# Kernel tuning notes

Measured on AMD Instinct MI355X. Metric: run time of the kernel, lower is better.

Reference implementation:

```python
import jax, jax.numpy as jnp
import numpy as np

D = 768
H = 8
DH = D // H
SCALE = DH ** -0.5


def layer_norm(x, g, b, eps=1e-5):
    mu = jnp.mean(x, axis=-1, keepdims=True)
    var = jnp.var(x, axis=-1, keepdims=True)
    return (x - mu) * jax.lax.rsqrt(var + eps) * g + b


def setup_inputs() -> dict:
    key = jax.random.key(0)
    ks = jax.random.split(key, 8)
    B, N = 8, 1024
    s = lambda fan_in: 1.0 / np.sqrt(fan_in)
    return {
        "x": jax.random.normal(ks[0], (B, N, D), jnp.float32),
        "w_qkv": jax.random.normal(ks[1], (D, 3 * D), jnp.float32) * s(D),
        "w_o": jax.random.normal(ks[2], (D, D), jnp.float32) * s(D),
        "b_o": jnp.zeros((D,), jnp.float32),
        "w1": jax.random.normal(ks[3], (D, 4 * D), jnp.float32) * s(D),
        "b1": jnp.zeros((4 * D,), jnp.float32),
        "w2": jax.random.normal(ks[4], (4 * D, D), jnp.float32) * s(4 * D),
        "b2": jnp.zeros((D,), jnp.float32),
        "g1": jnp.ones((D,), jnp.float32), "be1": jnp.zeros((D,), jnp.float32),
        "gm": jnp.ones((D,), jnp.float32), "bm": jnp.zeros((D,), jnp.float32),
        "g3": jnp.ones((D,), jnp.float32), "be3": jnp.zeros((D,), jnp.float32),
    }


def reference(x, w_qkv, w_o, b_o, w1, b1, w2, b2, g1, be1, gm, bm, g3, be3):
    B, N, _ = x.shape
    # --- attention branch (pre-norm) ---
    h = layer_norm(x, g1, be1)
    qkv = h @ w_qkv                                   # (B,N,3D)
    qkv = qkv.reshape(B, N, 3, H, DH).transpose(2, 0, 3, 1, 4)  # (3,B,H,N,Dh)
    q, k, v = qkv[0], qkv[1], qkv[2]
    att = jax.nn.softmax(jnp.einsum('bhnd,bhmd->bhnm', q, k) * SCALE, axis=-1)
    o = jnp.einsum('bhnm,bhmd->bhnd', att, v)         # (B,H,N,Dh)
    # faithful to original: reshape WITHOUT transposing heads back
    o = o.reshape(B, N, D)
    o = o @ w_o + b_o
    x = o + x
    # --- MLP branch (has its own pre-norm; GELU after BOTH linears; dropout off) ---
    h = layer_norm(x, gm, bm)
    h = jax.nn.gelu(h @ w1 + b1, approximate=False)
    h = jax.nn.gelu(h @ w2 + b2, approximate=False)
    x = h + x
    return layer_norm(x, g3, be3)
```

## Files before the change

### kernel.cpp

```cpp
#include <hip/hip_runtime.h>
#include <cmath>
#include <cstdint>

typedef __bf16 bf16;
typedef __bf16 bf16x8 __attribute__((ext_vector_type(8)));
typedef __bf16 bf16x4 __attribute__((ext_vector_type(4)));
typedef float  f32x4  __attribute__((ext_vector_type(4)));

#define M_TOK 8192
#define SCALE_ 0.10206207261596575f

__device__ __forceinline__ void gld_lds16(const void* g, void* l) {
  __builtin_amdgcn_global_load_lds(
      (__attribute__((address_space(1))) void*)(uintptr_t)g,
      (__attribute__((address_space(3))) void*)(uintptr_t)l,
      16, 0, 0);
}

__device__ __forceinline__ float gelu_f(float x) {
  float u = x * (0.7978845608f + 0.0356774081f * x * x);
  float t = 1.0f - 2.0f / (__expf(2.0f * u) + 1.0f);
  return 0.5f * x * (1.0f + t);
}

__global__ __launch_bounds__(256) void make_frags_kernel(
    const float* __restrict__ w_qkv, const float* __restrict__ w_o,
    const float* __restrict__ w1, const float* __restrict__ w2,
    bf16* __restrict__ fqkv, bf16* __restrict__ fwo, bf16* __restrict__ fw1,
    bf16* __restrict__ fw2) {
  int chunk = blockIdx.x * 4 + (threadIdx.x >> 6);
  int lane = threadIdx.x & 63;
  const float* src;
  bf16* dst;
  int K, N, base;
  if (chunk < 3456) {
    src = w_qkv; dst = fqkv; K = 768; N = 2304; base = 0;
  } else if (chunk < 4608) {
    src = w_o; dst = fwo; K = 768; N = 768; base = 3456;
  } else if (chunk < 9216) {
    src = w1; dst = fw1; K = 768; N = 3072; base = 4608;
  } else {
    src = w2; dst = fw2; K = 3072; N = 768; base = 9216;
  }
  int lid = chunk - base;
  int kc = K / 32;
  int n16 = lid / kc, c = lid - n16 * kc;
  int lr = lane & 15, qd = lane >> 4;
  int n = n16 * 16 + lr;
  int k0 = c * 32 + qd * 8;
  bf16x8 v;
#pragma unroll
  for (int e = 0; e < 8; e++) v[e] = (bf16)src[(size_t)(k0 + e) * N + n];
  *(bf16x8*)&dst[(size_t)lid * 512 + lane * 8] = v;
}

__global__ __launch_bounds__(256) void ln_kernel(
    const float* __restrict__ x, const float* __restrict__ g,
    const float* __restrict__ b, bf16* __restrict__ ob) {
  int w = threadIdx.x >> 6, lane = threadIdx.x & 63;
  size_t row = (size_t)blockIdx.x * 4 + w;
  const float* xr = x + row * 768;
  float4 v[3];
  float s = 0.f, sq = 0.f;
#pragma unroll
  for (int k = 0; k < 3; k++) {
    v[k] = *(const float4*)(xr + (k * 64 + lane) * 4);
    s += v[k].x + v[k].y + v[k].z + v[k].w;
    sq += v[k].x * v[k].x + v[k].y * v[k].y + v[k].z * v[k].z + v[k].w * v[k].w;
  }
#pragma unroll
  for (int off = 32; off >= 1; off >>= 1) {
    s += __shfl_xor(s, off);
    sq += __shfl_xor(sq, off);
  }
  float mean = s * (1.f / 768.f);
  float rstd = rsqrtf(sq * (1.f / 768.f) - mean * mean + 1e-5f);
#pragma unroll
  for (int k = 0; k < 3; k++) {
    int c = (k * 64 + lane) * 4;
    float4 gg = *(const float4*)(g + c);
    float4 bb = *(const float4*)(b + c);
    bf16x4 pk = {(bf16)((v[k].x - mean) * rstd * gg.x + bb.x),
                 (bf16)((v[k].y - mean) * rstd * gg.y + bb.y),
                 (bf16)((v[k].z - mean) * rstd * gg.z + bb.z),
                 (bf16)((v[k].w - mean) * rstd * gg.w + bb.w)};
    *(bf16x4*)(ob + row * 768 + c) = pk;
  }
}

__global__ __launch_bounds__(256) void ln2_reduce_kernel(
    const bf16* __restrict__ p, const float* __restrict__ bo,
    const float* __restrict__ xres, const float* __restrict__ g,
    const float* __restrict__ b, bf16* __restrict__ x2,
    bf16* __restrict__ h2) {
  int w = threadIdx.x >> 6, lane = threadIdx.x & 63;
  size_t row = (size_t)blockIdx.x * 4 + w;
  const bf16* p0 = p + row * 768;
  const bf16* p1 = p0 + (size_t)M_TOK * 768;
  const float* xr = xres + row * 768;
  float4 v[3];
  float s = 0.f, sq = 0.f;
#pragma unroll
  for (int k = 0; k < 3; k++) {
    int c = (k * 64 + lane) * 4;
    bf16x4 a0 = *(const bf16x4*)(p0 + c);
    bf16x4 a1 = *(const bf16x4*)(p1 + c);
    float4 bb = *(const float4*)(bo + c);
    float4 rr = *(const float4*)(xr + c);
    v[k].x = (float)a0[0] + (float)a1[0] + bb.x + rr.x;
    v[k].y = (float)a0[1] + (float)a1[1] + bb.y + rr.y;
    v[k].z = (float)a0[2] + (float)a1[2] + bb.z + rr.z;
    v[k].w = (float)a0[3] + (float)a1[3] + bb.w + rr.w;
    bf16x4 xo = {(bf16)v[k].x, (bf16)v[k].y, (bf16)v[k].z, (bf16)v[k].w};
    *(bf16x4*)(x2 + row * 768 + c) = xo;
    s += v[k].x + v[k].y + v[k].z + v[k].w;
    sq += v[k].x * v[k].x + v[k].y * v[k].y + v[k].z * v[k].z + v[k].w * v[k].w;
  }
#pragma unroll
  for (int off = 32; off >= 1; off >>= 1) {
    s += __shfl_xor(s, off);
    sq += __shfl_xor(sq, off);
  }
  float mean = s * (1.f / 768.f);
  float rstd = rsqrtf(sq * (1.f / 768.f) - mean * mean + 1e-5f);
#pragma unroll
  for (int k = 0; k < 3; k++) {
    int c = (k * 64 + lane) * 4;
    float4 gg = *(const float4*)(g + c);
    float4 bb = *(const float4*)(b + c);
    bf16x4 pk = {(bf16)((v[k].x - mean) * rstd * gg.x + bb.x),
                 (bf16)((v[k].y - mean) * rstd * gg.y + bb.y),
                 (bf16)((v[k].z - mean) * rstd * gg.z + bb.z),
                 (bf16)((v[k].w - mean) * rstd * gg.w + bb.w)};
    *(bf16x4*)(h2 + row * 768 + c) = pk;
  }
}

__global__ __launch_bounds__(256) void ln3_reduce_kernel(
    const bf16* __restrict__ p, const float* __restrict__ b2,
    const bf16* __restrict__ x2, const float* __restrict__ g,
    const float* __restrict__ b, float* __restrict__ out) {
  int w = threadIdx.x >> 6, lane = threadIdx.x & 63;
  size_t row = (size_t)blockIdx.x * 4 + w;
  const bf16* p0 = p + row * 768;
  const bf16* p1 = p0 + (size_t)M_TOK * 768;
  const bf16* xr = x2 + row * 768;
  float4 v[3];
  float s = 0.f, sq = 0.f;
#pragma unroll
  for (int k = 0; k < 3; k++) {
    int c = (k * 64 + lane) * 4;
    bf16x4 a0 = *(const bf16x4*)(p0 + c);
    bf16x4 a1 = *(const bf16x4*)(p1 + c);
    float4 bb = *(const float4*)(b2 + c);
    bf16x4 rr = *(const bf16x4*)(xr + c);
    v[k].x = gelu_f((float)a0[0] + (float)a1[0] + bb.x) + (float)rr[0];
    v[k].y = gelu_f((float)a0[1] + (float)a1[1] + bb.y) + (float)rr[1];
    v[k].z = gelu_f((float)a0[2] + (float)a1[2] + bb.z) + (float)rr[2];
    v[k].w = gelu_f((float)a0[3] + (float)a1[3] + bb.w) + (float)rr[3];
    s += v[k].x + v[k].y + v[k].z + v[k].w;
    sq += v[k].x * v[k].x + v[k].y * v[k].y + v[k].z * v[k].z + v[k].w * v[k].w;
  }
#pragma unroll
  for (int off = 32; off >= 1; off >>= 1) {
    s += __shfl_xor(s, off);
    sq += __shfl_xor(sq, off);
  }
  float mean = s * (1.f / 768.f);
  float rstd = rsqrtf(sq * (1.f / 768.f) - mean * mean + 1e-5f);
#pragma unroll
  for (int k = 0; k < 3; k++) {
    int c = (k * 64 + lane) * 4;
    float4 gg = *(const float4*)(g + c);
    float4 bb = *(const float4*)(b + c);
    float4 ov = {(v[k].x - mean) * rstd * gg.x + bb.x,
                 (v[k].y - mean) * rstd * gg.y + bb.y,
                 (v[k].z - mean) * rstd * gg.z + bb.z,
                 (v[k].w - mean) * rstd * gg.w + bb.w};
    *(float4*)(out + row * 768 + c) = ov;
  }
}

template <int EPI, int LDA, int KTOT, int KSL, int NN>
__global__ __launch_bounds__(512, 2) void gemm8p_kernel(
    const bf16* __restrict__ A, const bf16* __restrict__ Bf,
    const float* __restrict__ bias, bf16* __restrict__ outb,
    bf16* __restrict__ qo, bf16* __restrict__ ko, bf16* __restrict__ vto) {
  constexpr int KCg = KTOT / 32;
  constexpr int NT = KSL / 64;
  __shared__ __align__(16) bf16 smem[3][24576];
  int tid = threadIdx.x;
  int w = tid >> 6, l = tid & 63;
  int qd = l >> 4, lr = l & 15;
  int bm0 = blockIdx.x * 128, bn0 = blockIdx.y * 256;
  int kbase = blockIdx.z * KSL;
  int wm = (w >> 2) * 64;
  int wnl = (w & 3) * 4;

  int rA = w * 8 + (l >> 3);
  int csA = (l & 7) ^ (l >> 3);
  const bf16* pA =
      A + (size_t)(bm0 + rA) * LDA + kbase + csA * 8;
  const bf16* pB0 =
      Bf + ((size_t)((bn0 >> 4) + (w >> 1)) * KCg + (kbase >> 5) + (w & 1)) *
               512 +
      l * 8;

  auto STG_A = [&](int t, bf16* buf) {
    gld_lds16(pA + t * 64, (char*)buf + w * 1024);
    gld_lds16(pA + t * 64 + (size_t)64 * LDA, (char*)buf + (8 + w) * 1024);
  };
  auto STG_B = [&](int t, bf16* buf, int g) {
    gld_lds16(pB0 + (size_t)g * (4 * KCg * 512) + (size_t)t * 1024,
              (char*)buf + 16384 + (w + 8 * g) * 1024);
  };

  STG_A(0, smem[0]);
  STG_B(0, smem[0], 0); STG_B(0, smem[0], 1);
  STG_B(0, smem[0], 2); STG_B(0, smem[0], 3);
  STG_A(1, smem[1]);
  STG_B(1, smem[1], 0); STG_B(1, smem[1], 1);
  STG_B(1, smem[1], 2); STG_B(1, smem[1], 3);
  asm volatile("s_waitcnt vmcnt(6)" ::: "memory");
  __builtin_amdgcn_sched_barrier(0);
  __builtin_amdgcn_s_barrier();

  f32x4 acc[4][4] = {};

#pragma unroll 1
  for (int kt3 = 0; kt3 < NT; kt3 += 3) {
#pragma unroll
    for (int u = 0; u < 3; ++u) {
      const int kt = kt3 + u;
      const bf16* Ab = smem[u];
      const bf16* Bb = smem[u] + 8192;
      bf16* nbuf = smem[(u + 2) % 3];
      bool st = (kt + 2) < NT;
#pragma unroll
      for (int k2 = 0; k2 < 2; ++k2) {
        bf16x8 af[4], bv[4];
#pragma unroll
        for (int i = 0; i < 4; ++i)
          af[i] = *(const bf16x8*)(Ab + (wm + i * 16 + lr) * 64 +
                                   (((k2 << 2) | qd) ^ (lr & 7)) * 8);
#pragma unroll
        for (int j = 0; j < 4; ++j)
          bv[j] = *(const bf16x8*)(Bb + (((wnl + j) << 1) | k2) * 512 + l * 8);
        if (k2 == 0) {
          if (st) { STG_A(kt + 2, nbuf); STG_B(kt + 2, nbuf, 0); }
        } else {
          if (st) {
            STG_B(kt + 2, nbuf, 1);
            STG_B(kt + 2, nbuf, 2);
            STG_B(kt + 2, nbuf, 3);
          }
        }
        __builtin_amdgcn_s_barrier();
        asm volatile("s_waitcnt lgkmcnt(0)" ::: "memory");
        __builtin_amdgcn_sched_barrier(0);
        __builtin_amdgcn_s_setprio(1);
#pragma unroll
        for (int i = 0; i < 4; ++i)
#pragma unroll
          for (int j = 0; j < 4; ++j)
            acc[i][j] = __builtin_amdgcn_mfma_f32_16x16x32_bf16(
                af[i], bv[j], acc[i][j], 0, 0, 0);
        __builtin_amdgcn_s_setprio(0);
      }
      if (kt + 1 < NT) {
        if (st) asm volatile("s_waitcnt vmcnt(6)" ::: "memory");
        else    asm volatile("s_waitcnt vmcnt(0)" ::: "memory");
        __builtin_amdgcn_sched_barrier(0);
        __builtin_amdgcn_s_barrier();
      }
    }
  }

  int wn = (w & 3) * 64;
  bf16* outbs = (EPI == 5) ? outb + (size_t)blockIdx.z * M_TOK * NN : outb;

#pragma unroll
  for (int i = 0; i < 4; i++) {
#pragma unroll
    for (int j = 0; j < 4; j++) {
      if (EPI == 4) {
        int colt = bn0 + wn + j * 16;
        int which = colt / 768;
        int rem = colt - which * 768;
        int h = rem / 96;
        int dhb = rem - h * 96;
        int row0 = bm0 + wm + i * 16 + qd * 4;
        int b = row0 >> 10, n0 = row0 & 1023;
        int bh = b * 8 + h;
        if (which == 2) {
          bf16x4 pk = {(bf16)acc[i][j][0], (bf16)acc[i][j][1],
                       (bf16)acc[i][j][2], (bf16)acc[i][j][3]};
          *(bf16x4*)(vto + ((size_t)(bh * 96 + dhb + lr)) * 1024 + n0) = pk;
        } else if (which == 0) {
#pragma unroll
          for (int r = 0; r < 4; r++)
            qo[((size_t)bh * 1024 + n0 + r) * 96 + dhb + lr] =
                (bf16)(acc[i][j][r] * SCALE_);
        } else {
#pragma unroll
          for (int r = 0; r < 4; r++)
            ko[((size_t)bh * 1024 + n0 + r) * 96 + dhb + lr] =
                (bf16)acc[i][j][r];
        }
      } else {
#pragma unroll
        for (int r = 0; r < 4; r++) {
          int row = bm0 + wm + i * 16 + qd * 4 + r;
          int col = bn0 + wn + j * 16 + lr;
          size_t o = (size_t)row * NN + col;
          float v = acc[i][j][r];
          if (EPI == 2) {
            outbs[o] = (bf16)gelu_f(v + bias[col]);
          } else {
            outbs[o] = (bf16)v;
          }
        }
      }
    }
  }
}

__global__ __launch_bounds__(256) void attn_kernel(
    const bf16* __restrict__ qb, const bf16* __restrict__ kb,
    const bf16* __restrict__ vtb, bf16* __restrict__ operm) {
  __shared__ __align__(16) bf16 Ks[2][64 * 104];
  __shared__ __align__(16) bf16 Vs[2][96 * 72];
  __shared__ __align__(16) bf16 Ps[128 * 72];
  int t = threadIdx.x;
  int w = t >> 6, lane = t & 63;
  int qd = lane >> 4, lr = lane & 15;
  int bh = blockIdx.x, nt0 = blockIdx.y * 128;
  int bq = bh >> 3, hh = bh & 7;

  const bf16* kgb = kb + (size_t)bh * 1024 * 96;
  const bf16* vgb = vtb + (size_t)bh * 96 * 1024;

  bf16x8 kreg[3], vreg[3];
#pragma unroll
  for (int it = 0; it < 3; it++) {
    int idx = it * 256 + t;
    kreg[it] = *(const bf16x8*)(kgb + (idx / 12) * 96 + (idx % 12) * 8);
    vreg[it] = *(const bf16x8*)(vgb + (size_t)(idx >> 3) * 1024 + (idx & 7) * 8);
  }

  const bf16* qg = qb + ((size_t)bh * 1024 + nt0 + w * 32) * 96;
  bf16x8 afq[2][3];
#pragma unroll
  for (int i = 0; i < 2; i++)
#pragma unroll
    for (int ks = 0; ks < 3; ks++)
      afq[i][ks] = *(const bf16x8*)(qg + (i * 16 + lr) * 96 + ks * 32 + qd * 8);

  f32x4 oacc[2][6] = {};
  float lst[2][4] = {};

  int cur = 0;
  for (int kt = 0; kt < 16; kt++) {
#pragma unroll
    for (int it = 0; it < 3; it++) {
      int idx = it * 256 + t;
      *(bf16x8*)&Ks[cur][(idx / 12) * 104 + (idx % 12) * 8] = kreg[it];
      *(bf16x8*)&Vs[cur][(idx >> 3) * 72 + (idx & 7) * 8] = vreg[it];
    }
    if (kt < 15) {
      const bf16* kg = kgb + (size_t)(kt + 1) * 64 * 96;
      const bf16* vg = vgb + (kt + 1) * 64;
#pragma unroll
      for (int it = 0; it < 3; it++) {
        int idx = it * 256 + t;
        kreg[it] = *(const bf16x8*)(kg + (idx / 12) * 96 + (idx % 12) * 8);
        vreg[it] =
            *(const bf16x8*)(vg + (size_t)(idx >> 3) * 1024 + (idx & 7) * 8);
      }
    }
    __syncthreads();

    f32x4 sacc[2][4] = {};
#pragma unroll
    for (int ks = 0; ks < 3; ks++) {
      bf16x8 bk[4];
#pragma unroll
      for (int jn = 0; jn < 4; jn++)
        bk[jn] =
            *(const bf16x8*)&Ks[cur][(jn * 16 + lr) * 104 + ks * 32 + qd * 8];
#pragma unroll
      for (int i = 0; i < 2; i++)
#pragma unroll
        for (int jn = 0; jn < 4; jn++)
          sacc[i][jn] = __builtin_amdgcn_mfma_f32_16x16x32_bf16(
              afq[i][ks], bk[jn], sacc[i][jn], 0, 0, 0);
    }

#pragma unroll
    for (int i = 0; i < 2; i++)
#pragma unroll
      for (int jn = 0; jn < 4; jn++)
#pragma unroll
        for (int r = 0; r < 4; r++) {
          float p = __expf(sacc[i][jn][r]);
          lst[i][r] += p;
          Ps[(w * 32 + i * 16 + qd * 4 + r) * 72 + jn * 16 + lr] = (bf16)p;
        }

#pragma unroll
    for (int ks = 0; ks < 2; ks++) {
      bf16x8 ap[2];
#pragma unroll
      for (int i = 0; i < 2; i++)
        ap[i] =
            *(const bf16x8*)&Ps[(w * 32 + i * 16 + lr) * 72 + ks * 32 + qd * 8];
#pragma unroll
      for (int jn = 0; jn < 6; jn++) {
        bf16x8 bv =
            *(const bf16x8*)&Vs[cur][(jn * 16 + lr) * 72 + ks * 32 + qd * 8];
#pragma unroll
        for (int i = 0; i < 2; i++)
          oacc[i][jn] = __builtin_amdgcn_mfma_f32_16x16x32_bf16(
              ap[i], bv, oacc[i][jn], 0, 0, 0);
      }
    }
    cur ^= 1;
  }

#pragma unroll
  for (int i = 0; i < 2; i++)
#pragma unroll
    for (int r = 0; r < 4; r++) {
#pragma unroll
      for (int off = 1; off < 16; off <<= 1)
        lst[i][r] += __shfl_xor(lst[i][r], off);
    }

#pragma unroll
  for (int i = 0; i < 2; i++) {
#pragma unroll
    for (int r = 0; r < 4; r++) {
      float inv = 1.0f / lst[i][r];
      int n = nt0 + w * 32 + i * 16 + qd * 4 + r;
      size_t rowo = (size_t)bq * 1024 + hh * 128 + (n >> 3);
      int colb = 96 * (n & 7);
#pragma unroll
      for (int jn = 0; jn < 6; jn++)
        operm[rowo * 768 + colb + jn * 16 + lr] =
            (bf16)(oacc[i][jn][r] * inv);
    }
  }
}

extern "C" void kernel_launch(void* const* d_in, const int* in_sizes, int n_in,
                              void* d_out, int out_size, void* d_ws,
                              size_t ws_size, hipStream_t stream) {
  const float* x = (const float*)d_in[0];
  const float* w_qkv = (const float*)d_in[1];
  const float* w_o = (const float*)d_in[2];
  const float* b_o = (const float*)d_in[3];
  const float* w1 = (const float*)d_in[4];
  const float* b1 = (const float*)d_in[5];
  const float* w2 = (const float*)d_in[6];
  const float* b2 = (const float*)d_in[7];
  const float* g1 = (const float*)d_in[8];
  const float* be1 = (const float*)d_in[9];
  const float* gm = (const float*)d_in[10];
  const float* bm = (const float*)d_in[11];
  const float* g3 = (const float*)d_in[12];
  const float* be3 = (const float*)d_in[13];

  char* ws = (char*)d_ws;
  size_t off = 0;
  auto alloc = [&](size_t bytes) {
    char* p = ws + off;
    off += (bytes + 255) & ~(size_t)255;
    return p;
  };
  const size_t SZ_TOK_BF = (size_t)M_TOK * 768 * 2;
  bf16* fqkv = (bf16*)alloc((size_t)2304 * 768 * 2);
  bf16* fwo = (bf16*)alloc((size_t)768 * 768 * 2);
  bf16* fw1 = (bf16*)alloc((size_t)3072 * 768 * 2);
  bf16* fw2 = (bf16*)alloc((size_t)768 * 3072 * 2);
  bf16* hA = (bf16*)alloc(SZ_TOK_BF);
  bf16* qb = (bf16*)alloc(SZ_TOK_BF);
  bf16* kbuf = (bf16*)alloc(SZ_TOK_BF);
  bf16* vtb = (bf16*)alloc(SZ_TOK_BF);
  bf16* x2 = (bf16*)alloc(SZ_TOK_BF);
  char* G = alloc((size_t)M_TOK * 3072 * 2);
  bf16* operm = hA;
  bf16* h2 = hA;
  bf16* pWo = (bf16*)G;
  bf16* a1 = (bf16*)G;
  bf16* pW2 = hA;

  make_frags_kernel<<<3456, 256, 0, stream>>>(w_qkv, w_o, w1, w2, fqkv, fwo,
                                              fw1, fw2);

  ln_kernel<<<M_TOK / 4, 256, 0, stream>>>(x, g1, be1, hA);

  gemm8p_kernel<4, 768, 768, 768, 2304><<<dim3(64, 9), 512, 0, stream>>>(
      hA, fqkv, nullptr, nullptr, qb, kbuf, vtb);

  attn_kernel<<<dim3(64, 8), 256, 0, stream>>>(qb, kbuf, vtb, operm);

  gemm8p_kernel<5, 768, 768, 384, 768><<<dim3(64, 3, 2), 512, 0, stream>>>(
      operm, fwo, nullptr, pWo, nullptr, nullptr, nullptr);

  ln2_reduce_kernel<<<M_TOK / 4, 256, 0, stream>>>(pWo, b_o, x, gm, bm, x2, h2);

  gemm8p_kernel<2, 768, 768, 768, 3072><<<dim3(64, 12), 512, 0, stream>>>(
      h2, fw1, b1, a1, nullptr, nullptr, nullptr);

  gemm8p_kernel<5, 3072, 3072, 1536, 768><<<dim3(64, 3, 2), 512, 0, stream>>>(
      a1, fw2, nullptr, pW2, nullptr, nullptr, nullptr);

  ln3_reduce_kernel<<<M_TOK / 4, 256, 0, stream>>>(pW2, b2, x2, g3, be3,
                                                   (float*)d_out);
}
```

Before: 353.4 us.

## Replace 128x256 8-wave GEMM with 128x128 4-wave GEMM using K=32 stages

Rewrites the shared GEMM kernel to use 128x128 output tiles with 4 waves (256 threads) and 32-wide K stages held in a triple-buffered LDS ring, instead of 128x256 tiles with 8 waves and 64-wide K stages. Launch grids double along N. Smaller tiles and less LDS per block should raise occupancy (3 blocks per CU) and the number of blocks, which improves load balance on 256 CUs. The cost is lower data reuse per tile, more global traffic, and more barrier syncs per unit of K.

After: 323.9 us. 1.09x faster.

```diff
diff --git a/kernel.cpp b/kernel.cpp
--- a/kernel.cpp
+++ b/kernel.cpp
@@ -182,93 +182,77 @@
 }
 
 template <int EPI, int LDA, int KTOT, int KSL, int NN>
-__global__ __launch_bounds__(512, 2) void gemm8p_kernel(
+__global__ __launch_bounds__(256, 3) void gemm128_kernel(
     const bf16* __restrict__ A, const bf16* __restrict__ Bf,
     const float* __restrict__ bias, bf16* __restrict__ outb,
     bf16* __restrict__ qo, bf16* __restrict__ ko, bf16* __restrict__ vto) {
   constexpr int KCg = KTOT / 32;
-  constexpr int NT = KSL / 64;
-  __shared__ __align__(16) bf16 smem[3][24576];
+  constexpr int NT = KSL / 32;
+  __shared__ __align__(16) bf16 smem[3][8192];
   int tid = threadIdx.x;
   int w = tid >> 6, l = tid & 63;
   int qd = l >> 4, lr = l & 15;
-  int bm0 = blockIdx.x * 128, bn0 = blockIdx.y * 256;
-  int kbase = blockIdx.z * KSL;
-  int wm = (w >> 2) * 64;
-  int wnl = (w & 3) * 4;
-
-  int rA = w * 8 + (l >> 3);
-  int csA = (l & 7) ^ (l >> 3);
-  const bf16* pA =
-      A + (size_t)(bm0 + rA) * LDA + kbase + csA * 8;
-  const bf16* pB0 =
-      Bf + ((size_t)((bn0 >> 4) + (w >> 1)) * KCg + (kbase >> 5) + (w & 1)) *
-               512 +
-      l * 8;
-
-  auto STG_A = [&](int t, bf16* buf) {
-    gld_lds16(pA + t * 64, (char*)buf + w * 1024);
-    gld_lds16(pA + t * 64 + (size_t)64 * LDA, (char*)buf + (8 + w) * 1024);
+  int bm0 = blockIdx.x * 128, bn0 = blockIdx.y * 128;
+  int kb = blockIdx.z * KSL;
+  int wm = (w >> 1) * 64, wn = (w & 1) * 64;
+  int wnl = (w & 1) * 4;
+
+  const bf16* pA = A + (size_t)(bm0 + w * 32 + (l >> 2)) * LDA + kb +
+                   (((l & 3) ^ ((l >> 3) & 3)) * 8);
+  const bf16* pB =
+      Bf + ((size_t)((bn0 >> 4) + w * 2) * KCg + (kb >> 5)) * 512 + l * 8;
+
+  auto STG = [&](int t, int b) {
+    char* dA = (char*)smem[b] + w * 2048;
+    char* dB = (char*)smem[b] + 8192 + w * 2048;
+    gld_lds16(pA + t * 32, dA);
+    gld_lds16(pA + t * 32 + (size_t)16 * LDA, dA + 1024);
+    gld_lds16(pB + (size_t)t * 512, dB);
+    gld_lds16(pB + (size_t)KCg * 512 + (size_t)t * 512, dB + 1024);
   };
-  auto STG_B = [&](int t, bf16* buf, int g) {
-    gld_lds16(pB0 + (size_t)g * (4 * KCg * 512) + (size_t)t * 1024,
-              (char*)buf + 16384 + (w + 8 * g) * 1024);
+  auto LDF = [&](int b, bf16x8* af, bf16x8* bv) {
+    const bf16* Ab = smem[b];
+    const bf16* Bb = smem[b] + 4096;
+#pragma unroll
+    for (int i = 0; i < 4; ++i) {
+      int r = wm + i * 16 + lr;
+      af[i] = *(const bf16x8*)(Ab + r * 32 + ((qd ^ ((lr >> 1) & 3)) * 8));
+    }
+#pragma unroll
+    for (int j = 0; j < 4; ++j)
+      bv[j] = *(const bf16x8*)(Bb + (wnl + j) * 512 + l * 8);
   };
 
-  STG_A(0, smem[0]);
-  STG_B(0, smem[0], 0); STG_B(0, smem[0], 1);
-  STG_B(0, smem[0], 2); STG_B(0, smem[0], 3);
-  STG_A(1, smem[1]);
-  STG_B(1, smem[1], 0); STG_B(1, smem[1], 1);
-  STG_B(1, smem[1], 2); STG_B(1, smem[1], 3);
-  asm volatile("s_waitcnt vmcnt(6)" ::: "memory");
+  f32x4 acc[4][4] = {};
+
+  STG(0, 0);
+  STG(1, 1);
+  asm volatile("s_waitcnt vmcnt(4)" ::: "memory");
   __builtin_amdgcn_sched_barrier(0);
   __builtin_amdgcn_s_barrier();
 
-  f32x4 acc[4][4] = {};
-
 #pragma unroll 1
-  for (int kt3 = 0; kt3 < NT; kt3 += 3) {
+  for (int t3 = 0; t3 < NT; t3 += 3) {
 #pragma unroll
     for (int u = 0; u < 3; ++u) {
-      const int kt = kt3 + u;
-      const bf16* Ab = smem[u];
-      const bf16* Bb = smem[u] + 8192;
-      bf16* nbuf = smem[(u + 2) % 3];
-      bool st = (kt + 2) < NT;
-#pragma unroll
-      for (int k2 = 0; k2 < 2; ++k2) {
-        bf16x8 af[4], bv[4];
-#pragma unroll
-        for (int i = 0; i < 4; ++i)
-          af[i] = *(const bf16x8*)(Ab + (wm + i * 16 + lr) * 64 +
-                                   (((k2 << 2) | qd) ^ (lr & 7)) * 8);
+      const int t = t3 + u;
+      const bool st = (t + 2) < NT;
+      if (st) STG(t + 2, (u + 2) % 3);
+      __builtin_amdgcn_sched_barrier(0);
+      bf16x8 af[4], bv[4];
+      LDF(u, af, bv);
+      asm volatile("s_waitcnt lgkmcnt(0)" ::: "memory");
+      __builtin_amdgcn_sched_barrier(0);
+      __builtin_amdgcn_s_setprio(1);
+#pragma unroll
+      for (int i = 0; i < 4; ++i)
 #pragma unroll
         for (int j = 0; j < 4; ++j)
-          bv[j] = *(const bf16x8*)(Bb + (((wnl + j) << 1) | k2) * 512 + l * 8);
-        if (k2 == 0) {
-          if (st) { STG_A(kt + 2, nbuf); STG_B(kt + 2, nbuf, 0); }
-        } else {
-          if (st) {
-            STG_B(kt + 2, nbuf, 1);
-            STG_B(kt + 2, nbuf, 2);
-            STG_B(kt + 2, nbuf, 3);
-          }
-        }
-        __builtin_amdgcn_s_barrier();
-        asm volatile("s_waitcnt lgkmcnt(0)" ::: "memory");
-        __builtin_amdgcn_sched_barrier(0);
-        __builtin_amdgcn_s_setprio(1);
-#pragma unroll
-        for (int i = 0; i < 4; ++i)
-#pragma unroll
-          for (int j = 0; j < 4; ++j)
-            acc[i][j] = __builtin_amdgcn_mfma_f32_16x16x32_bf16(
-                af[i], bv[j], acc[i][j], 0, 0, 0);
-        __builtin_amdgcn_s_setprio(0);
-      }
-      if (kt + 1 < NT) {
-        if (st) asm volatile("s_waitcnt vmcnt(6)" ::: "memory");
+          acc[i][j] = __builtin_amdgcn_mfma_f32_16x16x32_bf16(
+              af[i], bv[j], acc[i][j], 0, 0, 0);
+      __builtin_amdgcn_s_setprio(0);
+      if (t + 1 < NT) {
+        if (st) asm volatile("s_waitcnt vmcnt(4)" ::: "memory");
         else    asm volatile("s_waitcnt vmcnt(0)" ::: "memory");
         __builtin_amdgcn_sched_barrier(0);
         __builtin_amdgcn_s_barrier();
@@ -276,7 +260,6 @@
     }
   }
 
-  int wn = (w & 3) * 64;
   bf16* outbs = (EPI == 5) ? outb + (size_t)blockIdx.z * M_TOK * NN : outb;
 
 #pragma unroll
@@ -499,20 +482,20 @@
 
   ln_kernel<<<M_TOK / 4, 256, 0, stream>>>(x, g1, be1, hA);
 
-  gemm8p_kernel<4, 768, 768, 768, 2304><<<dim3(64, 9), 512, 0, stream>>>(
+  gemm128_kernel<4, 768, 768, 768, 2304><<<dim3(64, 18), 256, 0, stream>>>(
       hA, fqkv, nullptr, nullptr, qb, kbuf, vtb);
 
   attn_kernel<<<dim3(64, 8), 256, 0, stream>>>(qb, kbuf, vtb, operm);
 
-  gemm8p_kernel<5, 768, 768, 384, 768><<<dim3(64, 3, 2), 512, 0, stream>>>(
+  gemm128_kernel<5, 768, 768, 384, 768><<<dim3(64, 6, 2), 256, 0, stream>>>(
       operm, fwo, nullptr, pWo, nullptr, nullptr, nullptr);
 
   ln2_reduce_kernel<<<M_TOK / 4, 256, 0, stream>>>(pWo, b_o, x, gm, bm, x2, h2);
 
-  gemm8p_kernel<2, 768, 768, 768, 3072><<<dim3(64, 12), 512, 0, stream>>>(
+  gemm128_kernel<2, 768, 768, 768, 3072><<<dim3(64, 24), 256, 0, stream>>>(
       h2, fw1, b1, a1, nullptr, nullptr, nullptr);
 
-  gemm8p_kernel<5, 3072, 3072, 1536, 768><<<dim3(64, 3, 2), 512, 0, stream>>>(
+  gemm128_kernel<5, 3072, 3072, 1536, 768><<<dim3(64, 6, 2), 256, 0, stream>>>(
       a1, fw2, nullptr, pW2, nullptr, nullptr, nullptr);
 
   ln3_reduce_kernel<<<M_TOK / 4, 256, 0, stream>>>(pW2, b2, x2, g3, be3,
```
